# Optimization experiments

Hardware: AMD Instinct MI355X
Metric: run time of the kernel (lower is better)

The kernel has to match this reference:

```python
import jax, jax.numpy as jnp
import numpy as np

B, C, H, W = 32, 384, 32, 32
NH = 4            # num_heads
CC = 192          # conv_channels = ceil(384/2)
HID = 1536        # mlp hidden = 4*dim
EPS = 1e-6


def _ln2d(x, w, b):
    # LayerNorm over channel axis of NCHW
    u = x.mean(1, keepdims=True)
    s = ((x - u) ** 2).mean(1, keepdims=True)
    return w[:, None, None] * ((x - u) * jax.lax.rsqrt(s + EPS)) + b[:, None, None]


def setup_inputs() -> dict:
    key = jax.random.key(0)
    ks = jax.random.split(key, 8)
    f = lambda k, shp, sc: jax.random.normal(k, shp, jnp.float32) * sc
    return {
        "x": f(ks[0], (B, C, H, W), 1.0),
        "conv_w": f(ks[1], (CC, 1, 3, 3), 0.1),
        "conv_b": jnp.zeros((CC,), jnp.float32),
        "nxca_w": jnp.ones((C,), jnp.float32),
        "nxca_b": jnp.zeros((C,), jnp.float32),
        "temp": jnp.ones((NH, 1, 1), jnp.float32),
        "qkv_w": f(ks[2], (3 * C, C), 0.05),
        "qkv_b": jnp.zeros((3 * C,), jnp.float32),
        "proj_w": f(ks[3], (C, C), 0.05),
        "proj_b": jnp.zeros((C,), jnp.float32),
        "norm_w": jnp.ones((C,), jnp.float32),
        "norm_b": jnp.zeros((C,), jnp.float32),
        "fc1_w": f(ks[4], (HID, C), 0.05),
        "fc1_b": jnp.zeros((HID,), jnp.float32),
        "fc2_w": f(ks[5], (C, HID), 0.05),
        "fc2_b": jnp.zeros((C,), jnp.float32),
        "gamma_xca": jnp.ones((C,), jnp.float32),
        "gamma": jnp.ones((C,), jnp.float32),
    }


def reference(x, conv_w, conv_b, nxca_w, nxca_b, temp, qkv_w, qkv_b,
              proj_w, proj_b, norm_w, norm_b, fc1_w, fc1_b, fc2_w, fc2_b,
              gamma_xca, gamma):
    b, c, h, w = x.shape
    n = h * w
    hd = c // NH
    # depthwise 3x3 conv on first CC channels (in-place in torch -> shortcut
    # taken AFTER the conv, faithfully reproduced here)
    xc = jax.lax.conv_general_dilated(
        x[:, :CC], conv_w, (1, 1), ((1, 1), (1, 1)), feature_group_count=CC
    ) + conv_b[None, :, None, None]
    x = jnp.concatenate([xc, x[:, CC:]], axis=1)
    shortcut = x
    # XCA branch
    y = _ln2d(x, nxca_w, nxca_b)
    yf = y.reshape(b, c, n).transpose(0, 2, 1)                       # [B,N,C]
    qkv = (yf @ qkv_w.T + qkv_b).reshape(b, n, 3, NH, hd).transpose(2, 0, 3, 1, 4)
    q, k, v = qkv[0], qkv[1], qkv[2]                                  # [B,h,N,hd]
    q = q / jnp.maximum(jnp.linalg.norm(q, axis=-1, keepdims=True), 1e-12)
    k = k / jnp.maximum(jnp.linalg.norm(k, axis=-1, keepdims=True), 1e-12)
    attn = jax.nn.softmax(jnp.einsum('bhnd,bhmd->bhnm', q, k) * temp, axis=-1)
    o = jnp.einsum('bhnm,bhmd->bhnd', attn, v).transpose(0, 2, 1, 3).reshape(b, n, c)
    o = (o @ proj_w.T + proj_b).transpose(0, 2, 1).reshape(b, c, h, w)
    x = shortcut + gamma_xca[None, :, None, None] * o
    # MLP branch
    shortcut2 = x
    z = _ln2d(x, norm_w, norm_b).transpose(0, 2, 3, 1).reshape(b, n, c)
    z = jax.nn.gelu(z @ fc1_w.T + fc1_b, approximate=False) @ fc2_w.T + fc2_b
    z = z.reshape(b, h, w, c).transpose(0, 3, 1, 2)
    return shortcut2 + gamma[None, :, None, None] * z
```

## Files before the change

### kernel.cpp

```cpp
#include <hip/hip_runtime.h>
#include <cstdint>

typedef unsigned short u16;
typedef unsigned int u32;
typedef unsigned long long u64;
typedef __attribute__((ext_vector_type(4))) float f32x4;
typedef __attribute__((ext_vector_type(16))) float f32x16;
typedef __attribute__((ext_vector_type(8))) __bf16 bf16x8;
typedef __attribute__((ext_vector_type(8))) u16 u16x8;
typedef __attribute__((ext_vector_type(4))) u32 u32x4;
typedef __attribute__((ext_vector_type(2))) int i32x2;

#define DEV __device__ __forceinline__

DEV u16 cvt16(float f) {
  __bf16 h = (__bf16)f;
  return __builtin_bit_cast(u16, h);
}
DEV u16 f2bf(float f) {
  u32 u = __builtin_bit_cast(u32, f);
  u += 0x7fffu + ((u >> 16) & 1u);
  return (u16)(u >> 16);
}
DEV float bflo2f(u32 packed) { return __builtin_bit_cast(float, packed << 16); }
DEV float bfhi2f(u32 packed) { return __builtin_bit_cast(float, packed & 0xffff0000u); }

DEV void g2l16(void* lds_wave_base, const void* gsrc) {
  __builtin_amdgcn_global_load_lds(
      (const __attribute__((address_space(1))) u32*)gsrc,
      (__attribute__((address_space(3))) u32*)lds_wave_base, 16, 0, 0);
}

DEV float gelu_tanh(float v) {
  float z = v * (0.7978845608f + 0.0356774081f * v * v);
  float e = __expf(2.0f * z);
  float th = 1.0f - 2.0f / (e + 1.0f);
  return 0.5f * v * (1.0f + th);
}

__global__ __launch_bounds__(256) void conv_k(const float* __restrict__ x,
                                              const float* __restrict__ cw,
                                              const float* __restrict__ cb,
                                              float* __restrict__ xc) {
  const int bc = blockIdx.x;
  const int c = bc % 384;
  const int p4 = threadIdx.x * 4;
  const float* xp = x + ((size_t)bc << 10);
  float* op = xc + ((size_t)bc << 10) + p4;
  if (c >= 192) {
    *(f32x4*)op = *(const f32x4*)(xp + p4);
    return;
  }
  const int hh = p4 >> 5, ww0 = p4 & 31;
  const float* wb = cw + c * 9;
  float b0 = cb[c];
  float a0 = b0, a1 = b0, a2 = b0, a3 = b0;
#pragma unroll
  for (int dy = 0; dy < 3; ++dy) {
    int y = hh + dy - 1;
    if ((unsigned)y < 32u) {
      const float* rp = xp + y * 32 + ww0;
      f32x4 m = *(const f32x4*)rp;
      float lft = (ww0 > 0) ? rp[-1] : 0.f;
      float rgt = (ww0 < 28) ? rp[4] : 0.f;
      float w0 = wb[dy * 3], w1 = wb[dy * 3 + 1], w2 = wb[dy * 3 + 2];
      a0 += lft * w0 + m[0] * w1 + m[1] * w2;
      a1 += m[0] * w0 + m[1] * w1 + m[2] * w2;
      a2 += m[1] * w0 + m[2] * w1 + m[3] * w2;
      a3 += m[2] * w0 + m[3] * w1 + rgt * w2;
    }
  }
  f32x4 r = {a0, a1, a2, a3};
  *(f32x4*)op = r;
}

__global__ __launch_bounds__(256) void cvt4_k(const float* __restrict__ s0,
                                              const float* __restrict__ s1,
                                              const float* __restrict__ s2,
                                              const float* __restrict__ s3,
                                              u16* __restrict__ d0,
                                              u16* __restrict__ d1,
                                              u16* __restrict__ d2,
                                              u16* __restrict__ d3) {
  int id = blockIdx.x * 256 + threadIdx.x;
  if (id < 442368) d0[id] = f2bf(s0[id]);
  else if (id < 589824) d1[id - 442368] = f2bf(s1[id - 442368]);
  else if (id < 1179648) d2[id - 589824] = f2bf(s2[id - 589824]);
  else if (id < 1769472) d3[id - 1179648] = f2bf(s3[id - 1179648]);
}

__global__ __launch_bounds__(256) void ln_t_k(const float* __restrict__ X,
                                              const float* __restrict__ w,
                                              const float* __restrict__ bsh,
                                              u16* __restrict__ Y) {
  __shared__ float tile[384][33];
  __shared__ float ps[8][32], ps2[8][32];
  __shared__ float mean_s[32], rstd_s[32];
  const int b = blockIdx.y;
  const int p0 = blockIdx.x * 32;
  const int t = threadIdx.x;
  const int pl = t & 31, cg = t >> 5;
  const float* xb = X + (((size_t)b * 384) << 10) + p0 + pl;
  float s = 0.f, s2 = 0.f;
  for (int c = cg; c < 384; c += 8) {
    float v = xb[(size_t)c << 10];
    tile[c][pl] = v;
    s += v;
    s2 += v * v;
  }
  ps[cg][pl] = s;
  ps2[cg][pl] = s2;
  __syncthreads();
  if (t < 32) {
    float a = 0.f, a2 = 0.f;
#pragma unroll
    for (int g = 0; g < 8; ++g) { a += ps[g][t]; a2 += ps2[g][t]; }
    float mu = a * (1.f / 384.f);
    float var = a2 * (1.f / 384.f) - mu * mu;
    mean_s[t] = mu;
    rstd_s[t] = rsqrtf(var + 1e-6f);
  }
  __syncthreads();
  const int cl = t & 63, pg = t >> 6;
  for (int p = pg; p < 32; p += 4) {
    float mu = mean_s[p], rs = rstd_s[p];
    size_t orow = (((size_t)b << 10) + p0 + p) * 384;
#pragma unroll
    for (int cc = 0; cc < 6; ++cc) {
      int c = cc * 64 + cl;
      float v = (tile[c][p] - mu) * rs * w[c] + bsh[c];
      Y[orow + c] = f2bf(v);
    }
  }
}

__global__ __launch_bounds__(256) void normk_k(u16* __restrict__ QKV) {
  const int t = threadIdx.x;
  const int w = t >> 6, l = t & 63;
  const int rg = l >> 4, li = l & 15;
  const int tok = blockIdx.x * 16 + w * 4 + rg;
  u16* rowp = QKV + (size_t)tok * 1152 + 384;
#pragma unroll
  for (int h = 0; h < 4; ++h) {
    u16* p = rowp + h * 96 + li * 6;
    u32 a = *(const u32*)p;
    u32 b2 = *(const u32*)(p + 2);
    u32 c = *(const u32*)(p + 4);
    float v[6] = {bflo2f(a), bfhi2f(a), bflo2f(b2), bfhi2f(b2), bflo2f(c), bfhi2f(c)};
    float ss = 0.f;
#pragma unroll
    for (int i = 0; i < 6; ++i) ss += v[i] * v[i];
#pragma unroll
    for (int mk = 1; mk < 16; mk <<= 1) ss += __shfl_xor(ss, mk, 64);
    float sc = 1.0f / fmaxf(sqrtf(ss), 1e-12f);
    u32 o0 = (u32)f2bf(v[0] * sc) | ((u32)f2bf(v[1] * sc) << 16);
    u32 o1 = (u32)f2bf(v[2] * sc) | ((u32)f2bf(v[3] * sc) << 16);
    u32 o2 = (u32)f2bf(v[4] * sc) | ((u32)f2bf(v[5] * sc) << 16);
    *(u32*)p = o0;
    *(u32*)(p + 2) = o1;
    *(u32*)(p + 4) = o2;
  }
}

__global__ __launch_bounds__(256, 3) void attn_k(const u16* __restrict__ QKV,
                                                 const u16* __restrict__ Vg,
                                                 u16* __restrict__ O,
                                                 const float* __restrict__ temp) {
  __shared__ u16 Kt[2][6656];
  __shared__ u16 Vt[2][6144];
  const int t = threadIdx.x;
  const int w = t >> 6, l = t & 63;
  const int l31 = l & 31, hi = l >> 5;
  const int id = blockIdx.x;
  const int xcd = id & 7, jj = id >> 3;
  const int bh = xcd * 16 + (jj >> 3);
  const int qb = jj & 7;
  const int b = bh >> 2, h = bh & 3;
  const int q0 = qb * 128 + w * 32;
  const u16* Qb = QKV + (size_t)b * 1024 * 1152;
  const char* Kbg = (const char*)QKV + (size_t)b * 1024 * 2304 + 768 + 192 * h;
  const char* Vbg = (const char*)(Vg + (size_t)bh * 98304);
  const float tl2e = temp[h] * 1.44269504f;
  const float mT2 = -fabsf(temp[h]) * 1.44269504f;

  u32 kOff[4], vOff[3];
#pragma unroll
  for (int i = 0; i < 4; ++i) {
    int s = (i < 3) ? (i * 256 + t) : (768 + w * 16 + (l & 15));
    int row = s / 13, c = s - row * 13;
    kOff[i] = row * 2304 + ((c < 12) ? c * 16 : 0);
  }
#pragma unroll
  for (int i = 0; i < 3; ++i) {
    int s = i * 256 + t;
    int row = s >> 3, cb = (s & 7) * 16;
    vOff[i] = row * 2048 + (cb ^ ((row & 7) << 4));
  }

  bf16x8 qf[6];
  {
    const u16* qp = Qb + (size_t)(q0 + l31) * 1152 + h * 96 + hi * 8;
#pragma unroll
    for (int kc = 0; kc < 6; ++kc) qf[kc] = *(const bf16x8*)(qp + kc * 16);
  }
  float alpha;
  {
    float ss = 0.f;
#pragma unroll
    for (int kc = 0; kc < 6; ++kc)
#pragma unroll
      for (int e = 0; e < 8; ++e) {
        float v = (float)qf[kc][e];
        ss += v * v;
      }
    ss += __shfl_xor(ss, 32, 64);
    alpha = tl2e * rsqrtf(fmaxf(ss, 1e-24f));
  }

  f32x16 oa[3];
#pragma unroll
  for (int dt = 0; dt < 3; ++dt)
#pragma unroll
    for (int r = 0; r < 16; ++r) oa[dt][r] = 0.f;
  float l_r = 0.f;

#define STAGE(buf, kv0)                                                        \
  {                                                                            \
    const char* kb = Kbg + (size_t)(kv0) * 2304;                               \
    const char* vb = Vbg + (size_t)(kv0) * 2;                                  \
    char* kd = (char*)&Kt[buf][0];                                             \
    char* vd = (char*)&Vt[buf][0];                                             \
    g2l16(kd + w * 1024, kb + kOff[0]);                                        \
    g2l16(kd + 4096 + w * 1024, kb + kOff[1]);                                 \
    g2l16(kd + 8192 + w * 1024, kb + kOff[2]);                                 \
    if (l < 16) g2l16(kd + 12288 + w * 256, kb + kOff[3]);                     \
    g2l16(vd + w * 1024, vb + vOff[0]);                                        \
    g2l16(vd + 4096 + w * 1024, vb + vOff[1]);                                 \
    g2l16(vd + 8192 + w * 1024, vb + vOff[2]);                                 \
  }

  STAGE(0, 0);
  for (int tt = 0; tt < 16; ++tt) {
    const int cur = tt & 1;
    if (tt < 15) {
      STAGE(cur ^ 1, (tt + 1) * 64);
      asm volatile("s_waitcnt vmcnt(7)" ::: "memory");
    } else {
      asm volatile("s_waitcnt vmcnt(0)" ::: "memory");
    }
    __builtin_amdgcn_s_barrier();
    const char* Kc = (const char*)&Kt[cur][0];
    const char* Vc = (const char*)&Vt[cur][0];
    f32x16 st[2];
#pragma unroll
    for (int n = 0; n < 2; ++n)
#pragma unroll
      for (int r = 0; r < 16; ++r) st[n][r] = 0.f;
#pragma unroll
    for (int n = 0; n < 2; ++n) {
      const char* krow = Kc + (n * 32 + l31) * 208 + hi * 16;
#pragma unroll
      for (int kc = 0; kc < 6; ++kc) {
        bf16x8 kf = *(const bf16x8*)(krow + kc * 32);
        st[n] = __builtin_amdgcn_mfma_f32_32x32x16_bf16(kf, qf[kc], st[n], 0, 0, 0);
      }
    }
    u32 pk[2][8];
#pragma unroll
    for (int n = 0; n < 2; ++n) {
      float p[16];
#pragma unroll
      for (int r = 0; r < 16; ++r) {
        p[r] = exp2f(fmaf(st[n][r], alpha, mT2));
        l_r += p[r];
      }
#pragma unroll
      for (int m = 0; m < 8; ++m)
        pk[n][m] = (u32)cvt16(p[2 * m]) | ((u32)cvt16(p[2 * m + 1]) << 16);
    }
#pragma unroll
    for (int c = 0; c < 4; ++c) {
      const int n = c >> 1, cc = c & 1;
      i32x2 s1 = __builtin_amdgcn_permlane32_swap((int)pk[n][4 * cc],
                                                  (int)pk[n][4 * cc + 2], 0, 0);
      i32x2 s2 = __builtin_amdgcn_permlane32_swap((int)pk[n][4 * cc + 1],
                                                  (int)pk[n][4 * cc + 3], 0, 0);
      u32x4 wd;
      wd[0] = (u32)s1[0]; wd[1] = (u32)s2[0];
      wd[2] = (u32)s1[1]; wd[3] = (u32)s2[1];
      bf16x8 pa = __builtin_bit_cast(bf16x8, wd);
      const u32 vcol = (u32)((c * 32 + hi * 16) ^ ((l31 & 7) << 4));
#pragma unroll
      for (int dt = 0; dt < 3; ++dt) {
        bf16x8 vf = *(const bf16x8*)(Vc + (dt * 32 + l31) * 128 + vcol);
        oa[dt] = __builtin_amdgcn_mfma_f32_32x32x16_bf16(pa, vf, oa[dt], 0, 0, 0);
      }
    }
    __builtin_amdgcn_s_barrier();
  }
#undef STAGE
  l_r += __shfl_xor(l_r, 32, 64);
  float inv = 1.0f / l_r;
#pragma unroll
  for (int r = 0; r < 16; ++r) {
    const int qr = (r & 3) + 8 * (r >> 2) + 4 * hi;
    float invr = __shfl(inv, qr, 64);
    const int tok = q0 + qr;
    u16* orow = O + ((size_t)b * 1024 + tok) * 384 + h * 96;
#pragma unroll
    for (int dt = 0; dt < 3; ++dt)
      orow[dt * 32 + l31] = f2bf(oa[dt][r] * invr);
  }
}

template <int EPI>
__global__ __launch_bounds__(512) void gemm256_k(const u16* __restrict__ A,
                                                 const u16* __restrict__ B,
                                                 int N, int K,
                                                 const float* __restrict__ bias,
                                                 u16* __restrict__ vtp,
                                                 u16* __restrict__ outp,
                                                 int nbx) {
  __shared__ u16 SM[24576];
  const int t = threadIdx.x;
  const int w = t >> 6, l = t & 63;
  const int l15 = l & 15, kg = l >> 4;
  const int id = blockIdx.x;
  const int xcd = id & 7, jj = id >> 3;
  const int qq = jj / nbx;
  const int bx = jj - qq * nbx;
  const int by = xcd * 16 + qq;
  const int m0 = by * 256, n0 = bx * 128;
  const int wr = w >> 1, wc = w & 1;
  const size_t ldab = (size_t)K * 2;
  const char* pa1 = (const char*)A + (size_t)(m0 + (t >> 2)) * ldab + (t & 3) * 16;
  const char* pa2 = pa1 + (size_t)128 * ldab;
  const char* pb1 = (const char*)B + (size_t)(n0 + (t >> 2)) * ldab + (t & 3) * 16;
  char* SMc = (char*)SM;

  f32x4 acc[4][4];
#pragma unroll
  for (int m = 0; m < 4; ++m)
#pragma unroll
    for (int n = 0; n < 4; ++n) acc[m][n] = {0.f, 0.f, 0.f, 0.f};

  const int nkt = K >> 5;
  g2l16(SMc + w * 1024, pa1);
  g2l16(SMc + 8192 + w * 1024, pa2);
  g2l16(SMc + 32768 + w * 1024, pb1);
  for (int kt = 0; kt < nkt; ++kt) {
    const int buf = kt & 1;
    if (kt + 1 < nkt) {
      const size_t o = (size_t)(kt + 1) * 64;
      g2l16(SMc + (buf ^ 1) * 16384 + w * 1024, pa1 + o);
      g2l16(SMc + (buf ^ 1) * 16384 + 8192 + w * 1024, pa2 + o);
      g2l16(SMc + 32768 + (buf ^ 1) * 8192 + w * 1024, pb1 + o);
      asm volatile("s_waitcnt vmcnt(3)" ::: "memory");
    } else {
      asm volatile("s_waitcnt vmcnt(0)" ::: "memory");
    }
    __builtin_amdgcn_s_barrier();
    __builtin_amdgcn_sched_barrier(0);
    const u16* Ab = SM + buf * 8192;
    const u16* Bb = SM + 16384 + buf * 4096;
    bf16x8 af[4], bfr[4];
#pragma unroll
    for (int m = 0; m < 4; ++m)
      af[m] = *(const bf16x8*)(Ab + (wr * 64 + m * 16 + l15) * 32 + kg * 8);
#pragma unroll
    for (int n = 0; n < 4; ++n)
      bfr[n] = *(const bf16x8*)(Bb + (wc * 64 + n * 16 + l15) * 32 + kg * 8);
    __builtin_amdgcn_s_setprio(1);
#pragma unroll
    for (int m = 0; m < 4; ++m)
#pragma unroll
      for (int n = 0; n < 4; ++n)
        acc[m][n] = __builtin_amdgcn_mfma_f32_16x16x32_bf16(af[m], bfr[n], acc[m][n], 0, 0, 0);
    __builtin_amdgcn_s_setprio(0);
    __builtin_amdgcn_sched_barrier(0);
    __builtin_amdgcn_s_barrier();
  }

  if (EPI == 4 && n0 >= 768) {
#pragma unroll
    for (int m = 0; m < 4; ++m) {
      const int tokbase = m0 + wr * 64 + m * 16 + kg * 4;
      const int bb = tokbase >> 10, nb = tokbase & 1023;
#pragma unroll
      for (int n = 0; n < 4; ++n) {
        int within = n0 - 768 + wc * 64 + n * 16 + l15;
        int hh = within / 96;
        int dd = within - hh * 96;
        float bs = bias[768 + within];
        int bh = bb * 4 + hh;
        u64 pk = 0;
#pragma unroll
        for (int j = 0; j < 4; ++j)
          pk |= (u64)cvt16(acc[m][n][j] + bs) << (16 * j);
        *(u64*)(vtp + ((size_t)bh * 96 + dd) * 1024 + nb) = pk;
      }
    }
    return;
  }

  u16* Ct = SM;
  float bs[4];
#pragma unroll
  for (int n = 0; n < 4; ++n) bs[n] = bias[n0 + wc * 64 + n * 16 + l15];
  const size_t ostride = (EPI == 4) ? 1152 : (size_t)N;
#pragma unroll
  for (int p = 0; p < 2; ++p) {
    if ((wr >> 1) == p) {
      u16* cw_ = Ct + ((wr & 1) * 64 + kg * 4) * 128 + wc * 64 + l15;
#pragma unroll
      for (int m = 0; m < 4; ++m)
#pragma unroll
        for (int n = 0; n < 4; ++n)
#pragma unroll
          for (int j = 0; j < 4; ++j) {
            float v = acc[m][n][j] + bs[n];
            if (EPI == 1) v = gelu_tanh(v);
            cw_[(m * 16 + j) * 128 + n * 16] = cvt16(v);
          }
    }
    __syncthreads();
    const int row_l = t >> 2;
    const int colc = (t & 3) * 32;
    const u16* src = Ct + row_l * 128 + colc;
    u16* dst = outp + (size_t)(m0 + p * 128 + row_l) * ostride + n0 + colc;
#pragma unroll
    for (int c4 = 0; c4 < 4; ++c4)
      *(u16x8*)(dst + c4 * 8) = *(const u16x8*)(src + c4 * 8);
    __syncthreads();
  }
}

__global__ __launch_bounds__(256) void gemm_k(const u16* __restrict__ A,
                                              const u16* __restrict__ B,
                                              int K,
                                              const float* __restrict__ bias,
                                              const float* __restrict__ gamma,
                                              const float* __restrict__ res,
                                              float* __restrict__ outp) {
  __shared__ u16 SM[16384];
  const int t = threadIdx.x;
  const int w = t >> 6, l = t & 63;
  const int l15 = l & 15, kg = l >> 4;
  int id = blockIdx.x;
  int xcd = id & 7, jj = id >> 3;
  int by = jj % 3;
  int bx = (jj / 3) * 8 + xcd;
  const int m0 = by * 128, n0 = bx * 128;
  const int wr = w >> 1, wc = w & 1;

  const size_t ldab = (size_t)K * 2;
  const char* pa1 = (const char*)A + (size_t)(m0 + (t >> 2)) * ldab + (t & 3) * 16;
  const char* pa2 = pa1 + (size_t)64 * ldab;
  const char* pb1 = (const char*)B + (size_t)(n0 + (t >> 2)) * ldab + (t & 3) * 16;
  const char* pb2 = pb1 + (size_t)64 * ldab;
  char* SMc = (char*)SM;

  f32x4 acc[4][4];
#pragma unroll
  for (int m = 0; m < 4; ++m)
#pragma unroll
    for (int n = 0; n < 4; ++n) acc[m][n] = {0.f, 0.f, 0.f, 0.f};

  const int nkt = K >> 5;
  {
    char* ad = SMc + w * 1024;
    char* bd = SMc + 16384 + w * 1024;
    g2l16(ad, pa1); g2l16(ad + 4096, pa2);
    g2l16(bd, pb1); g2l16(bd + 4096, pb2);
  }
  for (int kt = 0; kt < nkt; ++kt) {
    const int buf = kt & 1;
    if (kt + 1 < nkt) {
      const size_t o = (size_t)(kt + 1) * 64;
      char* ad = SMc + (buf ^ 1) * 8192 + w * 1024;
      char* bd = SMc + 16384 + (buf ^ 1) * 8192 + w * 1024;
      g2l16(ad, pa1 + o); g2l16(ad + 4096, pa2 + o);
      g2l16(bd, pb1 + o); g2l16(bd + 4096, pb2 + o);
      asm volatile("s_waitcnt vmcnt(4)" ::: "memory");
    } else {
      asm volatile("s_waitcnt vmcnt(0)" ::: "memory");
    }
    __builtin_amdgcn_s_barrier();
    __builtin_amdgcn_sched_barrier(0);
    const u16* Ab = SM + buf * 4096;
    const u16* Bb = SM + 8192 + buf * 4096;
    bf16x8 af[4], bfr[4];
#pragma unroll
    for (int m = 0; m < 4; ++m)
      af[m] = *(const bf16x8*)(Ab + (wr * 64 + m * 16 + l15) * 32 + kg * 8);
#pragma unroll
    for (int n = 0; n < 4; ++n)
      bfr[n] = *(const bf16x8*)(Bb + (wc * 64 + n * 16 + l15) * 32 + kg * 8);
    __builtin_amdgcn_s_setprio(1);
#pragma unroll
    for (int m = 0; m < 4; ++m)
#pragma unroll
      for (int n = 0; n < 4; ++n)
        acc[m][n] = __builtin_amdgcn_mfma_f32_16x16x32_bf16(af[m], bfr[n], acc[m][n], 0, 0, 0);
    __builtin_amdgcn_s_setprio(0);
    __builtin_amdgcn_sched_barrier(0);
    __builtin_amdgcn_s_barrier();
  }

#pragma unroll
  for (int m = 0; m < 4; ++m) {
#pragma unroll
    for (int n = 0; n < 4; ++n) {
      int tok = n0 + wc * 64 + n * 16 + l15;
      int bb = tok >> 10, p = tok & 1023;
#pragma unroll
      for (int j = 0; j < 4; ++j) {
        int c = m0 + wr * 64 + m * 16 + kg * 4 + j;
        size_t addr = (((size_t)(bb * 384 + c)) << 10) + p;
        outp[addr] = res[addr] + gamma[c] * (acc[m][n][j] + bias[c]);
      }
    }
  }
}

extern "C" void kernel_launch(void* const* d_in, const int* in_sizes, int n_in,
                              void* d_out, int out_size, void* d_ws,
                              size_t ws_size, hipStream_t stream) {
  const float* x      = (const float*)d_in[0];
  const float* conv_w = (const float*)d_in[1];
  const float* conv_b = (const float*)d_in[2];
  const float* nxca_w = (const float*)d_in[3];
  const float* nxca_b = (const float*)d_in[4];
  const float* temp   = (const float*)d_in[5];
  const float* qkv_w  = (const float*)d_in[6];
  const float* qkv_b  = (const float*)d_in[7];
  const float* proj_w = (const float*)d_in[8];
  const float* proj_b = (const float*)d_in[9];
  const float* norm_w = (const float*)d_in[10];
  const float* norm_b = (const float*)d_in[11];
  const float* fc1_w  = (const float*)d_in[12];
  const float* fc1_b  = (const float*)d_in[13];
  const float* fc2_w  = (const float*)d_in[14];
  const float* fc2_b  = (const float*)d_in[15];
  const float* g_xca  = (const float*)d_in[16];
  const float* g_mlp  = (const float*)d_in[17];
  (void)in_sizes; (void)n_in; (void)out_size; (void)ws_size;

  char* ws = (char*)d_ws;
  float* xc  = (float*)(ws);
  u16* Y     = (u16*)(ws + 50331648);
  u16* QKVr  = (u16*)(ws + 75497472);
  u16* Vt    = (u16*)(ws + 150994944);
  u16* Obuf  = Y;
  u16* H1    = QKVr;
  u16* wq    = (u16*)(ws + 176160768);
  u16* wp    = (u16*)(ws + 177045504);
  u16* w1    = (u16*)(ws + 177340416);
  u16* w2    = (u16*)(ws + 178520064);

  cvt4_k<<<6912, 256, 0, stream>>>(qkv_w, proj_w, fc1_w, fc2_w, wq, wp, w1, w2);

  conv_k<<<12288, 256, 0, stream>>>(x, conv_w, conv_b, xc);
  ln_t_k<<<dim3(32, 32), 256, 0, stream>>>(xc, nxca_w, nxca_b, Y);
  gemm256_k<4><<<1152, 512, 0, stream>>>(Y, wq, 1152, 384, qkv_b, Vt, QKVr, 9);
  normk_k<<<2048, 256, 0, stream>>>(QKVr);
  attn_k<<<1024, 256, 0, stream>>>(QKVr, Vt, Obuf, temp);
  gemm_k<<<768, 256, 0, stream>>>(wp, Obuf, 384, proj_b, g_xca, xc, xc);
  ln_t_k<<<dim3(32, 32), 256, 0, stream>>>(xc, norm_w, norm_b, Y);
  gemm256_k<1><<<1536, 512, 0, stream>>>(Y, w1, 1536, 384, fc1_b, nullptr, H1, 12);
  gemm_k<<<768, 256, 0, stream>>>(w2, H1, 1536, fc2_b, g_mlp, xc, (float*)d_out);
}
```

Measured before the change: 396.1 us.

## Unify GEMM kernels into templated 256-thread kernel with larger per-wave tiles

Replaces the 512-thread 256x128 GEMM and the 256-thread 128x128 GEMM with one templated kernel using 4 waves. Each wave now computes a 128x64 (or 64x128) sub-tile with 8x4 MFMA fragments, so register reuse rises. The projection and fc2 GEMMs move to 128x256 tiles with half as many blocks. The epilogue LDS staging now uses a padded 132-element row stride to reduce bank conflicts, and s_setprio is dropped. The trade-off is more accumulator registers per thread, which lowers occupancy, and fewer blocks for the residual GEMMs.

```diff
diff --git a/kernel.cpp b/kernel.cpp
--- a/kernel.cpp
+++ b/kernel.cpp
@@ -8,6 +8,7 @@
 typedef __attribute__((ext_vector_type(16))) float f32x16;
 typedef __attribute__((ext_vector_type(8))) __bf16 bf16x8;
 typedef __attribute__((ext_vector_type(8))) u16 u16x8;
+typedef __attribute__((ext_vector_type(4))) u16 u16x4;
 typedef __attribute__((ext_vector_type(4))) u32 u32x4;
 typedef __attribute__((ext_vector_type(2))) int i32x2;
 
@@ -313,82 +314,117 @@
   }
 }
 
-template <int EPI>
-__global__ __launch_bounds__(512) void gemm256_k(const u16* __restrict__ A,
-                                                 const u16* __restrict__ B,
-                                                 int N, int K,
-                                                 const float* __restrict__ bias,
-                                                 u16* __restrict__ vtp,
-                                                 u16* __restrict__ outp,
-                                                 int nbx) {
-  __shared__ u16 SM[24576];
+template <int BM, int BN, int EPI>
+__global__ __launch_bounds__(256) void gemmU_k(const u16* __restrict__ A,
+                                               const u16* __restrict__ B,
+                                               int Nn, int K,
+                                               const float* __restrict__ bias,
+                                               u16* __restrict__ vtp,
+                                               void* __restrict__ outp,
+                                               const float* __restrict__ gamma,
+                                               const float* __restrict__ res,
+                                               int nbx) {
+  constexpr int FM = BM / 32, FN = BN / 32;
+  constexpr int nA = BM / 64, nB = BN / 64;
+  constexpr int ABUFB = BM * 64;
+  constexpr int BBUFB = BN * 64;
+  __shared__ u16 SM[(BM + BN) * 64];
   const int t = threadIdx.x;
   const int w = t >> 6, l = t & 63;
   const int l15 = l & 15, kg = l >> 4;
-  const int id = blockIdx.x;
-  const int xcd = id & 7, jj = id >> 3;
-  const int qq = jj / nbx;
-  const int bx = jj - qq * nbx;
-  const int by = xcd * 16 + qq;
-  const int m0 = by * 256, n0 = bx * 128;
   const int wr = w >> 1, wc = w & 1;
+  int bx, by;
+  {
+    int id = blockIdx.x;
+    int xcd = id & 7, jj = id >> 3;
+    if (EPI == 2) { by = jj % 3; bx = (jj / 3) * 8 + xcd; }
+    else { int qq = jj / nbx; bx = jj - qq * nbx; by = xcd * 16 + qq; }
+  }
+  const int m0 = by * BM, n0 = bx * BN;
   const size_t ldab = (size_t)K * 2;
-  const char* pa1 = (const char*)A + (size_t)(m0 + (t >> 2)) * ldab + (t & 3) * 16;
-  const char* pa2 = pa1 + (size_t)128 * ldab;
-  const char* pb1 = (const char*)B + (size_t)(n0 + (t >> 2)) * ldab + (t & 3) * 16;
+  const char* pa[nA];
+  const char* pb[nB];
+#pragma unroll
+  for (int i = 0; i < nA; ++i)
+    pa[i] = (const char*)A + (size_t)(m0 + i * 64 + (t >> 2)) * ldab + (t & 3) * 16;
+#pragma unroll
+  for (int i = 0; i < nB; ++i)
+    pb[i] = (const char*)B + (size_t)(n0 + i * 64 + (t >> 2)) * ldab + (t & 3) * 16;
   char* SMc = (char*)SM;
 
-  f32x4 acc[4][4];
-#pragma unroll
-  for (int m = 0; m < 4; ++m)
-#pragma unroll
-    for (int n = 0; n < 4; ++n) acc[m][n] = {0.f, 0.f, 0.f, 0.f};
+  f32x4 acc[FM][FN];
+#pragma unroll
+  for (int m = 0; m < FM; ++m)
+#pragma unroll
+    for (int n = 0; n < FN; ++n) acc[m][n] = {0.f, 0.f, 0.f, 0.f};
+
+#define STG(bf, kti)                                                           \
+  {                                                                            \
+    const size_t o = (size_t)(kti) * 64;                                       \
+    _Pragma("unroll") for (int i = 0; i < nA; ++i)                             \
+        g2l16(SMc + (bf) * ABUFB + i * 4096 + w * 1024, pa[i] + o);            \
+    _Pragma("unroll") for (int i = 0; i < nB; ++i)                             \
+        g2l16(SMc + 2 * ABUFB + (bf) * BBUFB + i * 4096 + w * 1024, pb[i] + o);\
+  }
 
   const int nkt = K >> 5;
-  g2l16(SMc + w * 1024, pa1);
-  g2l16(SMc + 8192 + w * 1024, pa2);
-  g2l16(SMc + 32768 + w * 1024, pb1);
+  STG(0, 0);
   for (int kt = 0; kt < nkt; ++kt) {
     const int buf = kt & 1;
     if (kt + 1 < nkt) {
-      const size_t o = (size_t)(kt + 1) * 64;
-      g2l16(SMc + (buf ^ 1) * 16384 + w * 1024, pa1 + o);
-      g2l16(SMc + (buf ^ 1) * 16384 + 8192 + w * 1024, pa2 + o);
-      g2l16(SMc + 32768 + (buf ^ 1) * 8192 + w * 1024, pb1 + o);
-      asm volatile("s_waitcnt vmcnt(3)" ::: "memory");
+      STG(buf ^ 1, kt + 1);
+      asm volatile("s_waitcnt vmcnt(6)" ::: "memory");
     } else {
       asm volatile("s_waitcnt vmcnt(0)" ::: "memory");
     }
     __builtin_amdgcn_s_barrier();
     __builtin_amdgcn_sched_barrier(0);
-    const u16* Ab = SM + buf * 8192;
-    const u16* Bb = SM + 16384 + buf * 4096;
-    bf16x8 af[4], bfr[4];
-#pragma unroll
-    for (int m = 0; m < 4; ++m)
-      af[m] = *(const bf16x8*)(Ab + (wr * 64 + m * 16 + l15) * 32 + kg * 8);
-#pragma unroll
-    for (int n = 0; n < 4; ++n)
-      bfr[n] = *(const bf16x8*)(Bb + (wc * 64 + n * 16 + l15) * 32 + kg * 8);
-    __builtin_amdgcn_s_setprio(1);
-#pragma unroll
-    for (int m = 0; m < 4; ++m)
-#pragma unroll
-      for (int n = 0; n < 4; ++n)
-        acc[m][n] = __builtin_amdgcn_mfma_f32_16x16x32_bf16(af[m], bfr[n], acc[m][n], 0, 0, 0);
-    __builtin_amdgcn_s_setprio(0);
+    const u16* Ab = SM + buf * (BM * 32);
+    const u16* Bb = SM + BM * 64 + buf * (BN * 32);
+    bf16x8 af[FM], bfv[FN];
+#pragma unroll
+    for (int m = 0; m < FM; ++m)
+      af[m] = *(const bf16x8*)(Ab + (wr * (BM / 2) + m * 16 + l15) * 32 + kg * 8);
+#pragma unroll
+    for (int n = 0; n < FN; ++n)
+      bfv[n] = *(const bf16x8*)(Bb + (wc * (BN / 2) + n * 16 + l15) * 32 + kg * 8);
+#pragma unroll
+    for (int m = 0; m < FM; ++m)
+#pragma unroll
+      for (int n = 0; n < FN; ++n)
+        acc[m][n] = __builtin_amdgcn_mfma_f32_16x16x32_bf16(af[m], bfv[n], acc[m][n], 0, 0, 0);
     __builtin_amdgcn_sched_barrier(0);
     __builtin_amdgcn_s_barrier();
   }
+#undef STG
+
+  if (EPI == 2) {
+    float* out = (float*)outp;
+#pragma unroll
+    for (int m = 0; m < FM; ++m) {
+#pragma unroll
+      for (int n = 0; n < FN; ++n) {
+        int tok = n0 + wc * (BN / 2) + n * 16 + l15;
+        int bb = tok >> 10, p = tok & 1023;
+#pragma unroll
+        for (int j = 0; j < 4; ++j) {
+          int c = m0 + wr * (BM / 2) + m * 16 + kg * 4 + j;
+          size_t addr = (((size_t)(bb * 384 + c)) << 10) + p;
+          out[addr] = res[addr] + gamma[c] * (acc[m][n][j] + bias[c]);
+        }
+      }
+    }
+    return;
+  }
 
   if (EPI == 4 && n0 >= 768) {
 #pragma unroll
-    for (int m = 0; m < 4; ++m) {
-      const int tokbase = m0 + wr * 64 + m * 16 + kg * 4;
+    for (int m = 0; m < FM; ++m) {
+      const int tokbase = m0 + wr * (BM / 2) + m * 16 + kg * 4;
       const int bb = tokbase >> 10, nb = tokbase & 1023;
 #pragma unroll
-      for (int n = 0; n < 4; ++n) {
-        int within = n0 - 768 + wc * 64 + n * 16 + l15;
+      for (int n = 0; n < FN; ++n) {
+        int within = n0 - 768 + wc * (BN / 2) + n * 16 + l15;
         int hh = within / 96;
         int dd = within - hh * 96;
         float bs = bias[768 + within];
@@ -403,122 +439,40 @@
     return;
   }
 
-  u16* Ct = SM;
-  float bs[4];
-#pragma unroll
-  for (int n = 0; n < 4; ++n) bs[n] = bias[n0 + wc * 64 + n * 16 + l15];
-  const size_t ostride = (EPI == 4) ? 1152 : (size_t)N;
-#pragma unroll
-  for (int p = 0; p < 2; ++p) {
-    if ((wr >> 1) == p) {
-      u16* cw_ = Ct + ((wr & 1) * 64 + kg * 4) * 128 + wc * 64 + l15;
-#pragma unroll
-      for (int m = 0; m < 4; ++m)
-#pragma unroll
-        for (int n = 0; n < 4; ++n)
-#pragma unroll
-          for (int j = 0; j < 4; ++j) {
-            float v = acc[m][n][j] + bs[n];
-            if (EPI == 1) v = gelu_tanh(v);
-            cw_[(m * 16 + j) * 128 + n * 16] = cvt16(v);
-          }
-    }
-    __syncthreads();
-    const int row_l = t >> 2;
-    const int colc = (t & 3) * 32;
-    const u16* src = Ct + row_l * 128 + colc;
-    u16* dst = outp + (size_t)(m0 + p * 128 + row_l) * ostride + n0 + colc;
-#pragma unroll
-    for (int c4 = 0; c4 < 4; ++c4)
-      *(u16x8*)(dst + c4 * 8) = *(const u16x8*)(src + c4 * 8);
-    __syncthreads();
-  }
-}
-
-__global__ __launch_bounds__(256) void gemm_k(const u16* __restrict__ A,
-                                              const u16* __restrict__ B,
-                                              int K,
-                                              const float* __restrict__ bias,
-                                              const float* __restrict__ gamma,
-                                              const float* __restrict__ res,
-                                              float* __restrict__ outp) {
-  __shared__ u16 SM[16384];
-  const int t = threadIdx.x;
-  const int w = t >> 6, l = t & 63;
-  const int l15 = l & 15, kg = l >> 4;
-  int id = blockIdx.x;
-  int xcd = id & 7, jj = id >> 3;
-  int by = jj % 3;
-  int bx = (jj / 3) * 8 + xcd;
-  const int m0 = by * 128, n0 = bx * 128;
-  const int wr = w >> 1, wc = w & 1;
-
-  const size_t ldab = (size_t)K * 2;
-  const char* pa1 = (const char*)A + (size_t)(m0 + (t >> 2)) * ldab + (t & 3) * 16;
-  const char* pa2 = pa1 + (size_t)64 * ldab;
-  const char* pb1 = (const char*)B + (size_t)(n0 + (t >> 2)) * ldab + (t & 3) * 16;
-  const char* pb2 = pb1 + (size_t)64 * ldab;
-  char* SMc = (char*)SM;
-
-  f32x4 acc[4][4];
-#pragma unroll
-  for (int m = 0; m < 4; ++m)
-#pragma unroll
-    for (int n = 0; n < 4; ++n) acc[m][n] = {0.f, 0.f, 0.f, 0.f};
-
-  const int nkt = K >> 5;
   {
-    char* ad = SMc + w * 1024;
-    char* bd = SMc + 16384 + w * 1024;
-    g2l16(ad, pa1); g2l16(ad + 4096, pa2);
-    g2l16(bd, pb1); g2l16(bd + 4096, pb2);
-  }
-  for (int kt = 0; kt < nkt; ++kt) {
-    const int buf = kt & 1;
-    if (kt + 1 < nkt) {
-      const size_t o = (size_t)(kt + 1) * 64;
-      char* ad = SMc + (buf ^ 1) * 8192 + w * 1024;
-      char* bd = SMc + 16384 + (buf ^ 1) * 8192 + w * 1024;
-      g2l16(ad, pa1 + o); g2l16(ad + 4096, pa2 + o);
-      g2l16(bd, pb1 + o); g2l16(bd + 4096, pb2 + o);
-      asm volatile("s_waitcnt vmcnt(4)" ::: "memory");
-    } else {
-      asm volatile("s_waitcnt vmcnt(0)" ::: "memory");
-    }
-    __builtin_amdgcn_s_barrier();
-    __builtin_amdgcn_sched_barrier(0);
-    const u16* Ab = SM + buf * 4096;
-    const u16* Bb = SM + 8192 + buf * 4096;
-    bf16x8 af[4], bfr[4];
-#pragma unroll
-    for (int m = 0; m < 4; ++m)
-      af[m] = *(const bf16x8*)(Ab + (wr * 64 + m * 16 + l15) * 32 + kg * 8);
-#pragma unroll
-    for (int n = 0; n < 4; ++n)
-      bfr[n] = *(const bf16x8*)(Bb + (wc * 64 + n * 16 + l15) * 32 + kg * 8);
-    __builtin_amdgcn_s_setprio(1);
-#pragma unroll
-    for (int m = 0; m < 4; ++m)
-#pragma unroll
-      for (int n = 0; n < 4; ++n)
-        acc[m][n] = __builtin_amdgcn_mfma_f32_16x16x32_bf16(af[m], bfr[n], acc[m][n], 0, 0, 0);
-    __builtin_amdgcn_s_setprio(0);
-    __builtin_amdgcn_sched_barrier(0);
-    __builtin_amdgcn_s_barrier();
-  }
-
-#pragma unroll
-  for (int m = 0; m < 4; ++m) {
-#pragma unroll
-    for (int n = 0; n < 4; ++n) {
-      int tok = n0 + wc * 64 + n * 16 + l15;
-      int bb = tok >> 10, p = tok & 1023;
-#pragma unroll
-      for (int j = 0; j < 4; ++j) {
-        int c = m0 + wr * 64 + m * 16 + kg * 4 + j;
-        size_t addr = (((size_t)(bb * 384 + c)) << 10) + p;
-        outp[addr] = res[addr] + gamma[c] * (acc[m][n][j] + bias[c]);
-      }
+    u16* Ct = SM;
+    float bs[FN];
+#pragma unroll
+    for (int n = 0; n < FN; ++n) bs[n] = bias[n0 + wc * (BN / 2) + n * 16 + l15];
+    const size_t ostride = (size_t)Nn;
+#pragma unroll
+    for (int p = 0; p < 2; ++p) {
+      if (wr == p) {
+#pragma unroll
+        for (int m = 0; m < FM; ++m)
+#pragma unroll
+          for (int n = 0; n < FN; ++n)
+#pragma unroll
+            for (int j = 0; j < 4; ++j) {
+              float v = acc[m][n][j] + bs[n];
+              if (EPI == 1) v = gelu_tanh(v);
+              Ct[(m * 16 + kg * 4 + j) * 132 + wc * 64 + n * 16 + l15] = cvt16(v);
+            }
+      }
+      __syncthreads();
+      const int row = t >> 1, colc = (t & 1) * 64;
+      const u16* src = Ct + row * 132 + colc;
+      u16* dst = (u16*)outp + (size_t)(m0 + p * 128 + row) * ostride + n0 + colc;
+#pragma unroll
+      for (int c8 = 0; c8 < 8; ++c8) {
+        u16x4 lo = *(const u16x4*)(src + c8 * 8);
+        u16x4 hi = *(const u16x4*)(src + c8 * 8 + 4);
+        u16x8 v_;
+        v_[0] = lo[0]; v_[1] = lo[1]; v_[2] = lo[2]; v_[3] = lo[3];
+        v_[4] = hi[0]; v_[5] = hi[1]; v_[6] = hi[2]; v_[7] = hi[3];
+        *(u16x8*)(dst + c8 * 8) = v_;
+      }
+      __syncthreads();
     }
   }
 }
@@ -562,11 +516,17 @@
 
   conv_k<<<12288, 256, 0, stream>>>(x, conv_w, conv_b, xc);
   ln_t_k<<<dim3(32, 32), 256, 0, stream>>>(xc, nxca_w, nxca_b, Y);
-  gemm256_k<4><<<1152, 512, 0, stream>>>(Y, wq, 1152, 384, qkv_b, Vt, QKVr, 9);
+  gemmU_k<256, 128, 4><<<1152, 256, 0, stream>>>(Y, wq, 1152, 384, qkv_b, Vt,
+                                                 QKVr, nullptr, nullptr, 9);
   normk_k<<<2048, 256, 0, stream>>>(QKVr);
   attn_k<<<1024, 256, 0, stream>>>(QKVr, Vt, Obuf, temp);
-  gemm_k<<<768, 256, 0, stream>>>(wp, Obuf, 384, proj_b, g_xca, xc, xc);
+  gemmU_k<128, 256, 2><<<384, 256, 0, stream>>>(wp, Obuf, 32768, 384, proj_b,
+                                                nullptr, xc, g_xca, xc, 0);
   ln_t_k<<<dim3(32, 32), 256, 0, stream>>>(xc, norm_w, norm_b, Y);
-  gemm256_k<1><<<1536, 512, 0, stream>>>(Y, w1, 1536, 384, fc1_b, nullptr, H1, 12);
-  gemm_k<<<768, 256, 0, stream>>>(w2, H1, 1536, fc2_b, g_mlp, xc, (float*)d_out);
-}
+  gemmU_k<256, 128, 1><<<1536, 256, 0, stream>>>(Y, w1, 1536, 384, fc1_b,
+                                                 nullptr, H1, nullptr, nullptr,
+                                                 12);
+  gemmU_k<128, 256, 2><<<384, 256, 0, stream>>>(w2, H1, 32768, 1536, fc2_b,
+                                                nullptr, (float*)d_out, g_mlp,
+                                                xc, 0);
+}
```

New measurement: 514.2 us. +29.8%, slower.

## Use square 256x256-tile GEMM kernel for fc1 with GELU epilogue

Applied to the files above, without the earlier changes.

Adds a new fc1 GEMM kernel that computes 256x256 output tiles with 8 waves, double-buffered LDS staging and a padded LDS epilogue. Blocks are mapped so each XCD handles a contiguous band of rows. It replaces the previous gemm256_k<1> launch, halving the grid and increasing data reuse per tile. In exchange, per-thread accumulator register pressure and LDS use are higher, which may reduce occupancy.

```diff
diff --git a/kernel.cpp b/kernel.cpp
--- a/kernel.cpp
+++ b/kernel.cpp
@@ -8,6 +8,7 @@
 typedef __attribute__((ext_vector_type(16))) float f32x16;
 typedef __attribute__((ext_vector_type(8))) __bf16 bf16x8;
 typedef __attribute__((ext_vector_type(8))) u16 u16x8;
+typedef __attribute__((ext_vector_type(4))) u16 u16x4;
 typedef __attribute__((ext_vector_type(4))) u32 u32x4;
 typedef __attribute__((ext_vector_type(2))) int i32x2;
 
@@ -435,6 +436,114 @@
   }
 }
 
+__global__ __launch_bounds__(512, 2) void gemmsq_k(const u16* __restrict__ A,
+                                                   const u16* __restrict__ B,
+                                                   int Nn, int K,
+                                                   const float* __restrict__ bias,
+                                                   u16* __restrict__ outp,
+                                                   int nbx) {
+  __shared__ u16 SM[36864];
+  const int t = threadIdx.x;
+  const int w = t >> 6, l = t & 63;
+  const int l15 = l & 15, kg = l >> 4;
+  const int wr = w >> 2, wc = w & 3;
+  const int id = blockIdx.x;
+  const int xcd = id & 7, jj = id >> 3;
+  const int qq = jj / nbx;
+  const int bx = jj - qq * nbx;
+  const int by = xcd * 16 + qq;
+  const int m0 = by * 256, n0 = bx * 256;
+  const size_t ldab = (size_t)K * 2;
+  const char* pa1 = (const char*)A + (size_t)(m0 + (t >> 2)) * ldab + (t & 3) * 16;
+  const char* pa2 = pa1 + (size_t)128 * ldab;
+  const char* pb1 = (const char*)B + (size_t)(n0 + (t >> 2)) * ldab + (t & 3) * 16;
+  const char* pb2 = pb1 + (size_t)128 * ldab;
+  char* SMc = (char*)SM;
+
+  f32x4 acc[8][4];
+#pragma unroll
+  for (int m = 0; m < 8; ++m)
+#pragma unroll
+    for (int n = 0; n < 4; ++n) acc[m][n] = {0.f, 0.f, 0.f, 0.f};
+
+#define QSTG(bf, kti)                                                          \
+  {                                                                            \
+    const size_t o = (size_t)(kti) * 64;                                       \
+    g2l16(SMc + (bf) * 16384 + w * 1024, pa1 + o);                             \
+    g2l16(SMc + (bf) * 16384 + 8192 + w * 1024, pa2 + o);                      \
+    g2l16(SMc + 32768 + (bf) * 16384 + w * 1024, pb1 + o);                     \
+    g2l16(SMc + 32768 + (bf) * 16384 + 8192 + w * 1024, pb2 + o);              \
+  }
+
+  const int nkt = K >> 5;
+  QSTG(0, 0);
+  for (int kt = 0; kt < nkt; ++kt) {
+    const int buf = kt & 1;
+    if (kt + 1 < nkt) {
+      QSTG(buf ^ 1, kt + 1);
+      asm volatile("s_waitcnt vmcnt(4)" ::: "memory");
+    } else {
+      asm volatile("s_waitcnt vmcnt(0)" ::: "memory");
+    }
+    __builtin_amdgcn_s_barrier();
+    __builtin_amdgcn_sched_barrier(0);
+    const u16* Ab = SM + buf * 8192;
+    const u16* Bb = SM + 16384 + buf * 8192;
+    bf16x8 af[8], bfv[4];
+#pragma unroll
+    for (int m = 0; m < 8; ++m)
+      af[m] = *(const bf16x8*)(Ab + (wr * 128 + m * 16 + l15) * 32 + kg * 8);
+#pragma unroll
+    for (int n = 0; n < 4; ++n)
+      bfv[n] = *(const bf16x8*)(Bb + (wc * 64 + n * 16 + l15) * 32 + kg * 8);
+    __builtin_amdgcn_s_setprio(1);
+#pragma unroll
+    for (int m = 0; m < 8; ++m)
+#pragma unroll
+      for (int n = 0; n < 4; ++n)
+        acc[m][n] = __builtin_amdgcn_mfma_f32_16x16x32_bf16(af[m], bfv[n], acc[m][n], 0, 0, 0);
+    __builtin_amdgcn_s_setprio(0);
+    __builtin_amdgcn_sched_barrier(0);
+    __builtin_amdgcn_s_barrier();
+  }
+#undef QSTG
+
+  u16* Ct = SM;
+  float bs[4];
+#pragma unroll
+  for (int n = 0; n < 4; ++n) bs[n] = bias[n0 + wc * 64 + n * 16 + l15];
+#pragma unroll
+  for (int p = 0; p < 2; ++p) {
+    if (wr == p) {
+      u16* cw_ = Ct + (kg * 4) * 260 + wc * 64 + l15;
+#pragma unroll
+      for (int m = 0; m < 8; ++m)
+#pragma unroll
+        for (int n = 0; n < 4; ++n)
+#pragma unroll
+          for (int j = 0; j < 4; ++j) {
+            float v = gelu_tanh(acc[m][n][j] + bs[n]);
+            cw_[(m * 16 + j) * 260 + n * 16] = cvt16(v);
+          }
+    }
+    __syncthreads();
+    const int row = t >> 2;
+    const int colc = (t & 3) * 64;
+    const u16* src = Ct + row * 260 + colc;
+    u16* dst = outp + (size_t)(m0 + p * 128 + row) * (size_t)Nn + n0 + colc;
+#pragma unroll
+    for (int c8 = 0; c8 < 8; ++c8) {
+      u16x4 lo = *(const u16x4*)(src + c8 * 8);
+      u16x4 hi = *(const u16x4*)(src + c8 * 8 + 4);
+      u16x8 v_;
+      v_[0] = lo[0]; v_[1] = lo[1]; v_[2] = lo[2]; v_[3] = lo[3];
+      v_[4] = hi[0]; v_[5] = hi[1]; v_[6] = hi[2]; v_[7] = hi[3];
+      *(u16x8*)(dst + c8 * 8) = v_;
+    }
+    __syncthreads();
+  }
+}
+
 __global__ __launch_bounds__(256) void gemm_k(const u16* __restrict__ A,
                                               const u16* __restrict__ B,
                                               int K,
@@ -567,6 +676,6 @@
   attn_k<<<1024, 256, 0, stream>>>(QKVr, Vt, Obuf, temp);
   gemm_k<<<768, 256, 0, stream>>>(wp, Obuf, 384, proj_b, g_xca, xc, xc);
   ln_t_k<<<dim3(32, 32), 256, 0, stream>>>(xc, norm_w, norm_b, Y);
-  gemm256_k<1><<<1536, 512, 0, stream>>>(Y, w1, 1536, 384, fc1_b, nullptr, H1, 12);
+  gemmsq_k<<<768, 512, 0, stream>>>(Y, w1, 1536, 384, fc1_b, H1, 6);
   gemm_k<<<768, 256, 0, stream>>>(w2, H1, 1536, fc2_b, g_mlp, xc, (float*)d_out);
 }
```

Result: slower. 424.3 us (+7.1%).

## Store GEMM LDS tiles in MFMA fragment order and vectorize weight conversion

Applied to the files above, without the earlier changes.

The GEMM kernels now load global rows so that each wave writes a 16-row by 32-k MFMA fragment contiguously into LDS. Each lane then reads its operand with a single linear 16-byte access at l*8, where before it used a row-strided address that could cause bank conflicts. The weight fp32-to-bf16 conversion kernel is also changed to process four elements per thread with vector loads and stores, using a quarter of the blocks. Global load coalescing changes, because each 64-byte row chunk is now split across lanes differently.

```diff
diff --git a/kernel.cpp b/kernel.cpp
--- a/kernel.cpp
+++ b/kernel.cpp
@@ -8,6 +8,7 @@
 typedef __attribute__((ext_vector_type(16))) float f32x16;
 typedef __attribute__((ext_vector_type(8))) __bf16 bf16x8;
 typedef __attribute__((ext_vector_type(8))) u16 u16x8;
+typedef __attribute__((ext_vector_type(4))) u16 u16x4;
 typedef __attribute__((ext_vector_type(4))) u32 u32x4;
 typedef __attribute__((ext_vector_type(2))) int i32x2;
 
@@ -82,11 +83,18 @@
                                               u16* __restrict__ d1,
                                               u16* __restrict__ d2,
                                               u16* __restrict__ d3) {
-  int id = blockIdx.x * 256 + threadIdx.x;
-  if (id < 442368) d0[id] = f2bf(s0[id]);
-  else if (id < 589824) d1[id - 442368] = f2bf(s1[id - 442368]);
-  else if (id < 1179648) d2[id - 589824] = f2bf(s2[id - 589824]);
-  else if (id < 1769472) d3[id - 1179648] = f2bf(s3[id - 1179648]);
+  int id = (blockIdx.x * 256 + threadIdx.x) * 4;
+  const float* s; u16* d; int off;
+  if (id < 442368) { s = s0; d = d0; off = 0; }
+  else if (id < 589824) { s = s1; d = d1; off = 442368; }
+  else if (id < 1179648) { s = s2; d = d2; off = 589824; }
+  else { s = s3; d = d3; off = 1179648; }
+  int i = id - off;
+  f32x4 v = *(const f32x4*)(s + i);
+  u16x4 o;
+#pragma unroll
+  for (int j = 0; j < 4; ++j) o[j] = f2bf(v[j]);
+  *(u16x4*)(d + i) = o;
 }
 
 __global__ __launch_bounds__(256) void ln_t_k(const float* __restrict__ X,
@@ -333,9 +341,9 @@
   const int m0 = by * 256, n0 = bx * 128;
   const int wr = w >> 1, wc = w & 1;
   const size_t ldab = (size_t)K * 2;
-  const char* pa1 = (const char*)A + (size_t)(m0 + (t >> 2)) * ldab + (t & 3) * 16;
-  const char* pa2 = pa1 + (size_t)128 * ldab;
-  const char* pb1 = (const char*)B + (size_t)(n0 + (t >> 2)) * ldab + (t & 3) * 16;
+  const char* pa1 = (const char*)A + (size_t)(m0 + (0 * 8 + w) * 16 + l15) * ldab + kg * 16;
+  const char* pa2 = (const char*)A + (size_t)(m0 + (1 * 8 + w) * 16 + l15) * ldab + kg * 16;
+  const char* pb1 = (const char*)B + (size_t)(n0 + (w >> 2) * 64 + (w & 3) * 16 + l15) * ldab + kg * 16;
   char* SMc = (char*)SM;
 
   f32x4 acc[4][4];
@@ -366,10 +374,10 @@
     bf16x8 af[4], bfr[4];
 #pragma unroll
     for (int m = 0; m < 4; ++m)
-      af[m] = *(const bf16x8*)(Ab + (wr * 64 + m * 16 + l15) * 32 + kg * 8);
+      af[m] = *(const bf16x8*)(Ab + (wr * 4 + m) * 512 + l * 8);
 #pragma unroll
     for (int n = 0; n < 4; ++n)
-      bfr[n] = *(const bf16x8*)(Bb + (wc * 64 + n * 16 + l15) * 32 + kg * 8);
+      bfr[n] = *(const bf16x8*)(Bb + (wc * 4 + n) * 512 + l * 8);
     __builtin_amdgcn_s_setprio(1);
 #pragma unroll
     for (int m = 0; m < 4; ++m)
@@ -454,10 +462,10 @@
   const int wr = w >> 1, wc = w & 1;
 
   const size_t ldab = (size_t)K * 2;
-  const char* pa1 = (const char*)A + (size_t)(m0 + (t >> 2)) * ldab + (t & 3) * 16;
-  const char* pa2 = pa1 + (size_t)64 * ldab;
-  const char* pb1 = (const char*)B + (size_t)(n0 + (t >> 2)) * ldab + (t & 3) * 16;
-  const char* pb2 = pb1 + (size_t)64 * ldab;
+  const char* pa1 = (const char*)A + (size_t)(m0 + (0 * 4 + w) * 16 + l15) * ldab + kg * 16;
+  const char* pa2 = (const char*)A + (size_t)(m0 + (1 * 4 + w) * 16 + l15) * ldab + kg * 16;
+  const char* pb1 = (const char*)B + (size_t)(n0 + (0 * 4 + w) * 16 + l15) * ldab + kg * 16;
+  const char* pb2 = (const char*)B + (size_t)(n0 + (1 * 4 + w) * 16 + l15) * ldab + kg * 16;
   char* SMc = (char*)SM;
 
   f32x4 acc[4][4];
@@ -492,10 +500,10 @@
     bf16x8 af[4], bfr[4];
 #pragma unroll
     for (int m = 0; m < 4; ++m)
-      af[m] = *(const bf16x8*)(Ab + (wr * 64 + m * 16 + l15) * 32 + kg * 8);
+      af[m] = *(const bf16x8*)(Ab + (wr * 4 + m) * 512 + l * 8);
 #pragma unroll
     for (int n = 0; n < 4; ++n)
-      bfr[n] = *(const bf16x8*)(Bb + (wc * 64 + n * 16 + l15) * 32 + kg * 8);
+      bfr[n] = *(const bf16x8*)(Bb + (wc * 4 + n) * 512 + l * 8);
     __builtin_amdgcn_s_setprio(1);
 #pragma unroll
     for (int m = 0; m < 4; ++m)
@@ -558,7 +566,7 @@
   u16* w1    = (u16*)(ws + 177340416);
   u16* w2    = (u16*)(ws + 178520064);
 
-  cvt4_k<<<6912, 256, 0, stream>>>(qkv_w, proj_w, fc1_w, fc2_w, wq, wp, w1, w2);
+  cvt4_k<<<1728, 256, 0, stream>>>(qkv_w, proj_w, fc1_w, fc2_w, wq, wp, w1, w2);
 
   conv_k<<<12288, 256, 0, stream>>>(x, conv_w, conv_b, xc);
   ln_t_k<<<dim3(32, 32), 256, 0, stream>>>(xc, nxca_w, nxca_b, Y);
```

Result: slower. 435.8 us (+10.0%).
